# Kernel optimization log

Hardware: AMD Instinct MI355X
Metric: run time of the kernel (lower is better)

Reference implementation:

```python
import jax, jax.numpy as jnp
import numpy as np

HK, HV, D, K = 32, 32, 128, 4   # key heads, value heads, head dim, conv kernel
B = 128                          # decoding batch (seq=1 per step)
QKV = (2 * HK + HV) * D          # 12288


def _l2norm(x, eps=1e-6):
    return x * jax.lax.rsqrt(jnp.sum(x * x, axis=-1, keepdims=True) + eps)


def setup_inputs() -> dict:
    key = jax.random.key(0)
    ks = jax.random.split(key, 8)
    return {
        "mixed_qkv": jax.random.normal(ks[0], (B, QKV), jnp.float32),
        "forget_gate": jax.random.normal(ks[1], (B, HV * D), jnp.float32),
        "beta": jax.random.normal(ks[2], (B, HV), jnp.float32),
        "conv_state": jax.random.normal(ks[3], (B, QKV, K - 1), jnp.float32),
        "conv_weights": jax.random.normal(ks[4], (QKV, K), jnp.float32) * 0.1,
        "ssm_state": jax.random.normal(ks[5], (B, HV, D, D), jnp.float32) * 0.1,
        "A_log": jax.random.normal(ks[6], (HV,), jnp.float32),
        "dt_bias": jax.random.normal(ks[7], (HV * D,), jnp.float32),
    }


def reference(mixed_qkv, forget_gate, beta, conv_state, conv_weights, ssm_state, A_log, dt_bias):
    # --- causal conv1d single-step update (causal_conv1d_update, silu, no bias) ---
    # window = [past K-1 inputs | current input] per channel
    window = jnp.concatenate([conv_state, mixed_qkv[:, :, None]], axis=2)  # [B, QKV, K]
    x = jax.nn.silu(jnp.einsum('bck,ck->bc', window, conv_weights))        # [B, QKV]

    # --- split q/k/v heads ---
    qkv = x.reshape(B, 2 * HK + HV, D)
    q, k, v = qkv[:, :HK], qkv[:, HK:2 * HK], qkv[:, 2 * HK:]

    # use_qk_l2norm_in_kernel=True; scale=None -> D**-0.5 folded into q
    q = _l2norm(q) * (D ** -0.5)
    k = _l2norm(k)

    # use_gate_in_kernel=True: fused KDA gate  g = -exp(A_log) * softplus(f + dt_bias)
    g = -jnp.exp(A_log)[None, :, None] * jax.nn.softplus(
        forget_gate.reshape(B, HV, D) + dt_bias.reshape(HV, D)[None]
    )  # [B, HV, D] log-decay per key dim
    b = jax.nn.sigmoid(beta)  # [B, HV] per-head write strength

    # --- gated delta-rule recurrent update (single decode step) ---
    S = ssm_state * jnp.exp(g)[..., None]                  # decay state along key dim
    kv_mem = jnp.einsum('bhk,bhkv->bhv', k, S)             # current memory readout
    delta = (v - kv_mem) * b[..., None]                    # delta-rule correction
    S = S + k[..., None] * delta[:, :, None, :]            # rank-1 state write
    o = jnp.einsum('bhk,bhkv->bhv', q, S)                  # [B, HV, D]
    return o
```

## Files before the change

### kernel.cpp

```cpp
#include <hip/hip_runtime.h>
#include <math.h>

#define NHK   32
#define NHV   32
#define DDIM  128
#define NB    128
#define QKVC  12288

__device__ __forceinline__ float sigmoid_f(float x) { return 1.0f / (1.0f + expf(-x)); }
__device__ __forceinline__ float silu_f(float x)    { return x * sigmoid_f(x); }
__device__ __forceinline__ float softplus_f(float x){ return (x > 20.0f) ? x : log1pf(expf(x)); }

__global__ __launch_bounds__(256)
void kda_decode_kernel(const float* __restrict__ mixed,
                       const float* __restrict__ fgate,
                       const float* __restrict__ beta,
                       const float* __restrict__ cstate,
                       const float* __restrict__ cweight,
                       const float* __restrict__ ssm,
                       const float* __restrict__ A_log,
                       const float* __restrict__ dt_bias,
                       float* __restrict__ out)
{
    const int bh  = blockIdx.x;
    const int b   = bh >> 5;
    const int h   = bh & 31;
    const int tid = threadIdx.x;

    __shared__ float red[3][256];
    __shared__ float w_q[DDIM];
    __shared__ float w_k[DDIM];
    __shared__ float v_s[DDIM];
    __shared__ float pq[8][DDIM];
    __shared__ float pk[8][DDIM];

    float xq = 0.f, xk = 0.f, xv = 0.f;
    if (tid < DDIM) {
        const int d  = tid;
        const int cq = h * DDIM + d;
        const int ck = (NHK + h) * DDIM + d;
        const int cv = (2 * NHK + h) * DDIM + d;
        const size_t boff3 = (size_t)b * QKVC * 3;
        const size_t boff1 = (size_t)b * QKVC;

        {
            const float* s = cstate + boff3 + (size_t)cq * 3;
            const float* w = cweight + (size_t)cq * 4;
            xq = silu_f(s[0]*w[0] + s[1]*w[1] + s[2]*w[2] + mixed[boff1 + cq]*w[3]);
        }
        {
            const float* s = cstate + boff3 + (size_t)ck * 3;
            const float* w = cweight + (size_t)ck * 4;
            xk = silu_f(s[0]*w[0] + s[1]*w[1] + s[2]*w[2] + mixed[boff1 + ck]*w[3]);
        }
        {
            const float* s = cstate + boff3 + (size_t)cv * 3;
            const float* w = cweight + (size_t)cv * 4;
            xv = silu_f(s[0]*w[0] + s[1]*w[1] + s[2]*w[2] + mixed[boff1 + cv]*w[3]);
        }
    }

    red[0][tid] = (tid < DDIM) ? xq * xq : 0.f;
    red[1][tid] = (tid < DDIM) ? xk * xk : 0.f;
    red[2][tid] = (tid < DDIM) ? xq * xk : 0.f;
    __syncthreads();
    for (int s = 128; s > 0; s >>= 1) {
        if (tid < s) {
            red[0][tid] += red[0][tid + s];
            red[1][tid] += red[1][tid + s];
            red[2][tid] += red[2][tid + s];
        }
        __syncthreads();
    }
    const float q2  = red[0][0];
    const float k2  = red[1][0];
    const float qkd = red[2][0];

    const float dscale = 0.08838834764831845f;
    const float rq = rsqrtf(q2 + 1e-6f);
    const float rk = rsqrtf(k2 + 1e-6f);
    const float qk = qkd * rq * rk * dscale;
    const float bsig = sigmoid_f(beta[b * NHV + h]);

    if (tid < DDIM) {
        const int d = tid;
        const float g  = -expf(A_log[h]) *
                         softplus_f(fgate[(size_t)b * (NHV * DDIM) + h * DDIM + d] +
                                    dt_bias[h * DDIM + d]);
        const float eg = expf(g);
        w_q[d] = xq * rq * dscale * eg;
        w_k[d] = xk * rk * eg;
        v_s[d] = xv;
    }
    __syncthreads();

    const float* Sb = ssm + (size_t)(b * NHV + h) * DDIM * DDIM;
    const int g8 = tid >> 5;
    const int v4 = (tid & 31) * 4;

    float4 accq = {0.f, 0.f, 0.f, 0.f};
    float4 acck = {0.f, 0.f, 0.f, 0.f};
    #pragma unroll
    for (int kk = 0; kk < 16; ++kk) {
        const int k = g8 * 16 + kk;
        const float4 s = *reinterpret_cast<const float4*>(Sb + (size_t)k * DDIM + v4);
        const float wq = w_q[k];
        const float wk = w_k[k];
        accq.x = fmaf(wq, s.x, accq.x); accq.y = fmaf(wq, s.y, accq.y);
        accq.z = fmaf(wq, s.z, accq.z); accq.w = fmaf(wq, s.w, accq.w);
        acck.x = fmaf(wk, s.x, acck.x); acck.y = fmaf(wk, s.y, acck.y);
        acck.z = fmaf(wk, s.z, acck.z); acck.w = fmaf(wk, s.w, acck.w);
    }
    pq[g8][v4 + 0] = accq.x; pq[g8][v4 + 1] = accq.y;
    pq[g8][v4 + 2] = accq.z; pq[g8][v4 + 3] = accq.w;
    pk[g8][v4 + 0] = acck.x; pk[g8][v4 + 1] = acck.y;
    pk[g8][v4 + 2] = acck.z; pk[g8][v4 + 3] = acck.w;
    __syncthreads();

    if (tid < DDIM) {
        float aq = 0.f, ak = 0.f;
        #pragma unroll
        for (int g = 0; g < 8; ++g) { aq += pq[g][tid]; ak += pk[g][tid]; }
        const float o = aq + qk * (v_s[tid] - ak) * bsig;
        out[(size_t)(b * NHV + h) * DDIM + tid] = o;
    }
}

extern "C" void kernel_launch(void* const* d_in, const int* in_sizes, int n_in,
                              void* d_out, int out_size, void* d_ws, size_t ws_size,
                              hipStream_t stream) {
    const float* mixed   = (const float*)d_in[0];
    const float* fgate   = (const float*)d_in[1];
    const float* beta    = (const float*)d_in[2];
    const float* cstate  = (const float*)d_in[3];
    const float* cweight = (const float*)d_in[4];
    const float* ssm     = (const float*)d_in[5];
    const float* A_log   = (const float*)d_in[6];
    const float* dt_bias = (const float*)d_in[7];
    float* out = (float*)d_out;

    kda_decode_kernel<<<NB * NHV, 256, 0, stream>>>(
        mixed, fgate, beta, cstate, cweight, ssm, A_log, dt_bias, out);
}
```

Measured before the change: 380.3 us.

## Prefetch SSM state into registers early and use wavefront shuffle reductions

All global loads, including the 64 KB per-head SSM state slice, are now issued at kernel start and held in registers (16 float4 per thread). This lets the state fetch overlap with the conv, normalisation and gate math instead of waiting behind several barriers. The shared-memory tree reduction with eight barriers is replaced by wave64 xor-shuffles plus a single cross-wave combine, and partial sums are stored to shared memory as float4. Holding 64 extra state registers per thread raises register pressure and may lower occupancy.

```diff
diff --git a/kernel.cpp b/kernel.cpp
--- a/kernel.cpp
+++ b/kernel.cpp
@@ -27,94 +27,100 @@
     const int h   = bh & 31;
     const int tid = threadIdx.x;
 
-    __shared__ float red[3][256];
-    __shared__ float w_q[DDIM];
-    __shared__ float w_k[DDIM];
-    __shared__ float v_s[DDIM];
-    __shared__ float pq[8][DDIM];
-    __shared__ float pk[8][DDIM];
+    __shared__ float w_q[DDIM], w_k[DDIM], v_s[DDIM];
+    __shared__ float pq[8][DDIM], pk[8][DDIM];
+    __shared__ float part[4][3];
+
+    float cs_q[3], cs_k[3], cs_v[3];
+    float4 cw_q = {0,0,0,0}, cw_k = {0,0,0,0}, cw_v = {0,0,0,0};
+    float mx_q = 0.f, mx_k = 0.f, mx_v = 0.f, fg = 0.f, dtb = 0.f;
+    cs_q[0]=cs_q[1]=cs_q[2]=0.f; cs_k[0]=cs_k[1]=cs_k[2]=0.f; cs_v[0]=cs_v[1]=cs_v[2]=0.f;
+
+    const float betav = beta[b * NHV + h];
+    const float alog  = A_log[h];
+
+    if (tid < DDIM) {
+        const int cq = h * DDIM + tid;
+        const int ck = (NHK + h) * DDIM + tid;
+        const int cv = (2 * NHK + h) * DDIM + tid;
+        const size_t b3 = (size_t)b * QKVC * 3;
+        const size_t b1 = (size_t)b * QKVC;
+
+        #pragma unroll
+        for (int j = 0; j < 3; ++j) {
+            cs_q[j] = cstate[b3 + (size_t)cq * 3 + j];
+            cs_k[j] = cstate[b3 + (size_t)ck * 3 + j];
+            cs_v[j] = cstate[b3 + (size_t)cv * 3 + j];
+        }
+        cw_q = *reinterpret_cast<const float4*>(cweight + (size_t)cq * 4);
+        cw_k = *reinterpret_cast<const float4*>(cweight + (size_t)ck * 4);
+        cw_v = *reinterpret_cast<const float4*>(cweight + (size_t)cv * 4);
+        mx_q = mixed[b1 + cq];
+        mx_k = mixed[b1 + ck];
+        mx_v = mixed[b1 + cv];
+        fg   = fgate[(size_t)b * (NHV * DDIM) + h * DDIM + tid];
+        dtb  = dt_bias[h * DDIM + tid];
+    }
+
+    const float* Sb = ssm + (size_t)bh * (DDIM * DDIM);
+    const int g8 = tid >> 5;
+    const int v4 = (tid & 31) * 4;
+    float4 sreg[16];
+    #pragma unroll
+    for (int kk = 0; kk < 16; ++kk)
+        sreg[kk] = *reinterpret_cast<const float4*>(Sb + (size_t)(g8 * 16 + kk) * DDIM + v4);
 
     float xq = 0.f, xk = 0.f, xv = 0.f;
     if (tid < DDIM) {
-        const int d  = tid;
-        const int cq = h * DDIM + d;
-        const int ck = (NHK + h) * DDIM + d;
-        const int cv = (2 * NHK + h) * DDIM + d;
-        const size_t boff3 = (size_t)b * QKVC * 3;
-        const size_t boff1 = (size_t)b * QKVC;
-
-        {
-            const float* s = cstate + boff3 + (size_t)cq * 3;
-            const float* w = cweight + (size_t)cq * 4;
-            xq = silu_f(s[0]*w[0] + s[1]*w[1] + s[2]*w[2] + mixed[boff1 + cq]*w[3]);
-        }
-        {
-            const float* s = cstate + boff3 + (size_t)ck * 3;
-            const float* w = cweight + (size_t)ck * 4;
-            xk = silu_f(s[0]*w[0] + s[1]*w[1] + s[2]*w[2] + mixed[boff1 + ck]*w[3]);
-        }
-        {
-            const float* s = cstate + boff3 + (size_t)cv * 3;
-            const float* w = cweight + (size_t)cv * 4;
-            xv = silu_f(s[0]*w[0] + s[1]*w[1] + s[2]*w[2] + mixed[boff1 + cv]*w[3]);
-        }
+        xq = silu_f(cs_q[0]*cw_q.x + cs_q[1]*cw_q.y + cs_q[2]*cw_q.z + mx_q*cw_q.w);
+        xk = silu_f(cs_k[0]*cw_k.x + cs_k[1]*cw_k.y + cs_k[2]*cw_k.z + mx_k*cw_k.w);
+        xv = silu_f(cs_v[0]*cw_v.x + cs_v[1]*cw_v.y + cs_v[2]*cw_v.z + mx_v*cw_v.w);
     }
 
-    red[0][tid] = (tid < DDIM) ? xq * xq : 0.f;
-    red[1][tid] = (tid < DDIM) ? xk * xk : 0.f;
-    red[2][tid] = (tid < DDIM) ? xq * xk : 0.f;
+    float a0 = xq * xq, a1 = xk * xk, a2 = xq * xk;
+    #pragma unroll
+    for (int off = 32; off; off >>= 1) {
+        a0 += __shfl_xor(a0, off);
+        a1 += __shfl_xor(a1, off);
+        a2 += __shfl_xor(a2, off);
+    }
+    const int wid = tid >> 6;
+    if ((tid & 63) == 0) { part[wid][0] = a0; part[wid][1] = a1; part[wid][2] = a2; }
     __syncthreads();
-    for (int s = 128; s > 0; s >>= 1) {
-        if (tid < s) {
-            red[0][tid] += red[0][tid + s];
-            red[1][tid] += red[1][tid + s];
-            red[2][tid] += red[2][tid + s];
-        }
-        __syncthreads();
-    }
-    const float q2  = red[0][0];
-    const float k2  = red[1][0];
-    const float qkd = red[2][0];
+    const float q2  = part[0][0] + part[1][0];
+    const float k2  = part[0][1] + part[1][1];
+    const float qkd = part[0][2] + part[1][2];
 
     const float dscale = 0.08838834764831845f;
     const float rq = rsqrtf(q2 + 1e-6f);
     const float rk = rsqrtf(k2 + 1e-6f);
     const float qk = qkd * rq * rk * dscale;
-    const float bsig = sigmoid_f(beta[b * NHV + h]);
+    const float bsig = sigmoid_f(betav);
 
     if (tid < DDIM) {
-        const int d = tid;
-        const float g  = -expf(A_log[h]) *
-                         softplus_f(fgate[(size_t)b * (NHV * DDIM) + h * DDIM + d] +
-                                    dt_bias[h * DDIM + d]);
+        const float g  = -expf(alog) * softplus_f(fg + dtb);
         const float eg = expf(g);
-        w_q[d] = xq * rq * dscale * eg;
-        w_k[d] = xk * rk * eg;
-        v_s[d] = xv;
+        w_q[tid] = xq * rq * dscale * eg;
+        w_k[tid] = xk * rk * eg;
+        v_s[tid] = xv;
     }
     __syncthreads();
-
-    const float* Sb = ssm + (size_t)(b * NHV + h) * DDIM * DDIM;
-    const int g8 = tid >> 5;
-    const int v4 = (tid & 31) * 4;
 
     float4 accq = {0.f, 0.f, 0.f, 0.f};
     float4 acck = {0.f, 0.f, 0.f, 0.f};
     #pragma unroll
     for (int kk = 0; kk < 16; ++kk) {
         const int k = g8 * 16 + kk;
-        const float4 s = *reinterpret_cast<const float4*>(Sb + (size_t)k * DDIM + v4);
         const float wq = w_q[k];
         const float wk = w_k[k];
+        const float4 s = sreg[kk];
         accq.x = fmaf(wq, s.x, accq.x); accq.y = fmaf(wq, s.y, accq.y);
         accq.z = fmaf(wq, s.z, accq.z); accq.w = fmaf(wq, s.w, accq.w);
         acck.x = fmaf(wk, s.x, acck.x); acck.y = fmaf(wk, s.y, acck.y);
         acck.z = fmaf(wk, s.z, acck.z); acck.w = fmaf(wk, s.w, acck.w);
     }
-    pq[g8][v4 + 0] = accq.x; pq[g8][v4 + 1] = accq.y;
-    pq[g8][v4 + 2] = accq.z; pq[g8][v4 + 3] = accq.w;
-    pk[g8][v4 + 0] = acck.x; pk[g8][v4 + 1] = acck.y;
-    pk[g8][v4 + 2] = acck.z; pk[g8][v4 + 3] = acck.w;
+    *reinterpret_cast<float4*>(&pq[g8][v4]) = accq;
+    *reinterpret_cast<float4*>(&pk[g8][v4]) = acck;
     __syncthreads();
 
     if (tid < DDIM) {
@@ -122,7 +128,7 @@
         #pragma unroll
         for (int g = 0; g < 8; ++g) { aq += pq[g][tid]; ak += pk[g][tid]; }
         const float o = aq + qk * (v_s[tid] - ak) * bsig;
-        out[(size_t)(b * NHV + h) * DDIM + tid] = o;
+        out[(size_t)bh * DDIM + tid] = o;
     }
 }
 
```

Result: no change. 386.1 us (+1.5%).
